# Optimization experiments

Hardware: AMD Instinct MI355X
Metric: run time of the kernel (lower is better)

Reference implementation:

```python
import jax, jax.numpy as jnp
import numpy as np
from jax import lax

B, T, D, U = 64, 2048, 512, 32


def setup_inputs() -> dict:
    key = jax.random.key(0)
    k1, k2, k3, k4 = jax.random.split(key, 4)
    x = jax.random.normal(k1, (B, T, D), dtype=jnp.float32)
    # sequence lengths in [1, T]
    nwords = jnp.maximum(jax.random.randint(k2, (B,), 0, T, dtype=jnp.int32), 1)
    kernel = jax.random.normal(k3, (D, U), dtype=jnp.float32) * 0.02
    chain_kernel = jax.random.normal(k4, (U, U), dtype=jnp.float32) * 0.02
    bias = jnp.zeros((U,), dtype=jnp.float32)
    return {"x": x, "nwords": nwords, "kernel": kernel,
            "chain_kernel": chain_kernel, "bias": bias}


def _crf_decode(logits, trans, lengths):
    """Viterbi decode. logits [B,T,U], trans [U,U], lengths [B] int.
    Returns (pred_ids [B,T] int32, best_score [B])."""
    Bb, Tt, Uu = logits.shape
    alpha0 = logits[:, 0]                       # [B,U]
    # valid[t-1, b] = (t < lengths[b]) for t = 1..T-1
    valid = (jnp.arange(1, Tt)[:, None] < lengths[None, :])  # [T-1, B]
    logits_rest = jnp.transpose(logits[:, 1:], (1, 0, 2))    # [T-1, B, U]
    tag_iota = jnp.arange(Uu, dtype=jnp.int32)

    def fwd_step(alpha, inp):
        logit_t, v = inp                        # [B,U], [B]
        scores = alpha[:, :, None] + trans[None, :, :]   # [B, U_prev, U_cur]
        bp = jnp.argmax(scores, axis=1).astype(jnp.int32)  # [B,U]
        new_alpha = jnp.max(scores, axis=1) + logit_t        # [B,U]
        new_alpha = jnp.where(v[:, None], new_alpha, alpha)
        bp = jnp.where(v[:, None], bp, tag_iota[None, :])    # identity at pads
        return new_alpha, bp

    final_alpha, bps = lax.scan(fwd_step, alpha0, (logits_rest, valid))
    # bps: [T-1, B, U]
    last_tag = jnp.argmax(final_alpha, axis=-1).astype(jnp.int32)  # [B]
    best_score = jnp.max(final_alpha, axis=-1)                     # [B]

    def back_step(tag, bp_t):
        prev_tag = jnp.take_along_axis(bp_t, tag[:, None], axis=1)[:, 0]
        return prev_tag, tag

    first_tag, tags_rest = lax.scan(back_step, last_tag, bps, reverse=True)
    # tags_rest[t-1] = tag at time t; first_tag = tag at time 0
    pred = jnp.concatenate([first_tag[None, :], tags_rest], axis=0)  # [T,B]
    return jnp.transpose(pred, (1, 0)), best_score


def reference(x, nwords, kernel, chain_kernel, bias):
    # dense projection (activation = linear, keras default)
    logits = jnp.einsum('btd,du->btu', x, kernel) + bias  # [B,T,U]
    pred_ids, best_score = _crf_decode(logits, chain_kernel, nwords)
    return pred_ids, best_score
```

## Files before the change

kernel.cpp:

```cpp
#include <hip/hip_runtime.h>

#define BB 64
#define TT 2048
#define DD 512
#define UU 32

#define NSEG 16
#define SEGLEN 128
#define SEGSH 7
#define NJ (NSEG - 1)

__device__ int g_ts[BB * NJ];
__device__ float g_c[BB * NJ];
__device__ float g_bound[BB * NSEG * 64];

__global__ __launch_bounds__(256) void k1_logits(const float* __restrict__ x,
                                                 const float* __restrict__ w,
                                                 const float* __restrict__ bias,
                                                 float* __restrict__ out) {
  __shared__ float xs[256 * 34];
  __shared__ float wsh[32 * 36];
  const int tid = threadIdx.x;
  const long row0 = (long)blockIdx.x * 256;
  const int tr = tid >> 2;
  const int tc = tid & 3;
  const int ubase = tc * 8;
  const int sr = tid >> 3;
  const int sc = (tid & 7) * 4;

  float acc[4][8];
#pragma unroll
  for (int i = 0; i < 4; ++i)
#pragma unroll
    for (int j = 0; j < 8; ++j) acc[i][j] = 0.0f;

  for (int kc = 0; kc < DD; kc += 32) {
#pragma unroll
    for (int p = 0; p < 8; ++p) {
      const int r = p * 32 + sr;
      const float4 v = *(const float4*)(x + (row0 + r) * DD + kc + sc);
      *(float2*)(&xs[r * 34 + sc]) = make_float2(v.x, v.y);
      *(float2*)(&xs[r * 34 + sc + 2]) = make_float2(v.z, v.w);
    }
    {
      const int k = tid >> 3;
      const int uu4 = (tid & 7) * 4;
      const float4 v = *(const float4*)(w + (size_t)(kc + k) * UU + uu4);
      *(float4*)(&wsh[k * 36 + uu4]) = v;
    }
    __syncthreads();
#pragma unroll
    for (int kp = 0; kp < 16; ++kp) {
      const int k = kp * 2;
      const float4 wa0 = *(const float4*)(&wsh[k * 36 + ubase]);
      const float4 wa1 = *(const float4*)(&wsh[k * 36 + ubase + 4]);
      const float4 wb0 = *(const float4*)(&wsh[(k + 1) * 36 + ubase]);
      const float4 wb1 = *(const float4*)(&wsh[(k + 1) * 36 + ubase + 4]);
      const float wva[8] = {wa0.x, wa0.y, wa0.z, wa0.w, wa1.x, wa1.y, wa1.z, wa1.w};
      const float wvb[8] = {wb0.x, wb0.y, wb0.z, wb0.w, wb1.x, wb1.y, wb1.z, wb1.w};
#pragma unroll
      for (int i = 0; i < 4; ++i) {
        const float2 xv2 = *(const float2*)(&xs[(tr + 64 * i) * 34 + k]);
#pragma unroll
        for (int j = 0; j < 8; ++j) acc[i][j] = fmaf(xv2.x, wva[j], acc[i][j]);
#pragma unroll
        for (int j = 0; j < 8; ++j) acc[i][j] = fmaf(xv2.y, wvb[j], acc[i][j]);
      }
    }
    __syncthreads();
  }
  float bv[8];
#pragma unroll
  for (int j = 0; j < 8; ++j) bv[j] = bias[ubase + j];
#pragma unroll
  for (int i = 0; i < 4; ++i) {
    const long row = row0 + tr + 64 * i;
    float4 o0, o1;
    o0.x = acc[i][0] + bv[0]; o0.y = acc[i][1] + bv[1];
    o0.z = acc[i][2] + bv[2]; o0.w = acc[i][3] + bv[3];
    o1.x = acc[i][4] + bv[4]; o1.y = acc[i][5] + bv[5];
    o1.z = acc[i][6] + bv[6]; o1.w = acc[i][7] + bv[7];
    *(float4*)(out + row * UU + ubase) = o0;
    *(float4*)(out + row * UU + ubase + 4) = o1;
  }
}


#define ROTF(S) \
  __int_as_float(__builtin_amdgcn_update_dpp(0, __float_as_int(P), 0x120 + (S), 0xF, 0xF, true))

#define K2_TREE                                                              \
    const float c0 = P + tvS[0];                                             \
    const float c1 = ROTF(1) + tvS[1];                                       \
    const float c2 = ROTF(2) + tvS[2];                                       \
    const float c3 = ROTF(3) + tvS[3];                                       \
    const float c4 = ROTF(4) + tvS[4];                                       \
    const float c5 = ROTF(5) + tvS[5];                                       \
    const float c6 = ROTF(6) + tvS[6];                                       \
    const float c7 = ROTF(7) + tvS[7];                                       \
    const float c8 = ROTF(8) + tvS[8];                                       \
    const float c9 = ROTF(9) + tvS[9];                                       \
    const float c10 = ROTF(10) + tvS[10];                                    \
    const float c11 = ROTF(11) + tvS[11];                                    \
    const float c12 = ROTF(12) + tvS[12];                                    \
    const float c13 = ROTF(13) + tvS[13];                                    \
    const float c14 = ROTF(14) + tvS[14];                                    \
    const float c15 = ROTF(15) + tvS[15];                                    \
    const float d0 = fmaxf(fmaxf(c0, c1), c2);                               \
    const float d1 = fmaxf(fmaxf(c3, c4), c5);                               \
    const float d2 = fmaxf(fmaxf(c6, c7), c8);                               \
    const float d3 = fmaxf(fmaxf(c9, c10), c11);                             \
    const float d4 = fmaxf(fmaxf(c12, c13), c14);                            \
    const float e0 = fmaxf(fmaxf(d0, d1), d2);                               \
    const float e1 = fmaxf(fmaxf(d3, d4), c15);                              \
    const float pm = fmaxf(e0, e1);

#if __has_builtin(__builtin_amdgcn_permlane32_swap) && __has_builtin(__builtin_amdgcn_permlane16_swap)
#define K2_HAVE_PERMLANE 1
typedef unsigned int v2u __attribute__((ext_vector_type(2)));

#define K2_FSTEP(tval, lg) do {                                              \
    K2_TREE                                                                  \
    v2u s32 = __builtin_amdgcn_permlane32_swap(__float_as_uint(pm),          \
                                               __float_as_uint(pm), false, false); \
    const float pd = fmaxf(__uint_as_float(s32.x), __uint_as_float(s32.y)) + (lg); \
    v2u s16 = __builtin_amdgcn_permlane16_swap(__float_as_uint(pd),          \
                                               __float_as_uint(pd), false, false); \
    const float cx = m16sel ? __uint_as_float(s16.x) : __uint_as_float(s16.y); \
    P = bit5v ? cx : pd;                                                     \
    base[(size_t)(tval) * UU + cstoS] = P;                                   \
  } while (0)

__device__ __forceinline__ float k2_mcomb(float P, const float* tvS) {
  K2_TREE
  v2u s32 = __builtin_amdgcn_permlane32_swap(__float_as_uint(pm),
                                             __float_as_uint(pm), false, false);
  return fmaxf(__uint_as_float(s32.x), __uint_as_float(s32.y));
}

#define K2_RUNSEG(A_, E_) do {                                               \
    int tcc = (A_);                                                          \
    _Pragma("unroll")                                                        \
    for (int i = 0; i < 16; ++i) {                                           \
      int r = (A_) + i; if (r > (E_)) r = (E_);                              \
      bufA[i] = base[(size_t)r * UU + tgtS];                                 \
    }                                                                        \
    _Pragma("unroll 1")                                                      \
    for (; tcc + 31 <= (E_); tcc += 32) {                                    \
      _Pragma("unroll")                                                      \
      for (int i = 0; i < 16; ++i) bufB[i] = base[(size_t)(tcc + 16 + i) * UU + tgtS]; \
      _Pragma("unroll")                                                      \
      for (int i = 0; i < 16; ++i) K2_FSTEP(tcc + i, bufA[i]);               \
      _Pragma("unroll")                                                      \
      for (int i = 0; i < 16; ++i) {                                         \
        int r = tcc + 32 + i; if (r > (E_)) r = (E_);                        \
        bufA[i] = base[(size_t)r * UU + tgtS];                               \
      }                                                                      \
      _Pragma("unroll")                                                      \
      for (int i = 0; i < 16; ++i) K2_FSTEP(tcc + 16 + i, bufB[i]);          \
    }                                                                        \
    const int rem = (E_) - tcc + 1;                                          \
    if (rem > 0) {                                                           \
      _Pragma("unroll")                                                      \
      for (int i = 0; i < 16; ++i) {                                         \
        int r = tcc + 16 + i; if (r > (E_)) r = (E_);                        \
        bufB[i] = base[(size_t)r * UU + tgtS];                               \
      }                                                                      \
      _Pragma("unroll")                                                      \
      for (int i = 0; i < 16; ++i) { if (i < rem) K2_FSTEP(tcc + i, bufA[i]); } \
      _Pragma("unroll")                                                      \
      for (int i = 0; i < 16; ++i) { if (16 + i < rem) K2_FSTEP(tcc + 16 + i, bufB[i]); } \
    }                                                                        \
  } while (0)
#endif

__global__ __launch_bounds__(64) void k2a_forward(float* __restrict__ lb,
                                                  const float* __restrict__ trans) {
  const int lane = threadIdx.x;
  const int q = lane & 15;
  const int bit4 = (lane >> 4) & 1;
  const int bit5v = (lane >> 5) & 1;
  const int hiS = bit4 ^ bit5v;
  const int tgtS = bit4 * 16 + q;
  const int cstoS = hiS * 16 + q;
  const int role = blockIdx.x >> 6;
  const int b = blockIdx.x & 63;

  const int probe = __builtin_amdgcn_update_dpp(0, q, 0x121, 0xF, 0xF, false);
  const bool dirp = (probe == ((q + 1) & 15));

  float tvS[16];
#pragma unroll
  for (int s = 0; s < 16; ++s) {
    const int rp = dirp ? ((q + s) & 15) : ((q - s) & 15);
    tvS[s] = trans[(hiS * 16 + rp) * UU + tgtS];
  }

  float* base = lb + (size_t)b * TT * UU;
  float bufA[16], bufB[16];

#ifdef K2_HAVE_PERMLANE
  v2u p32 = __builtin_amdgcn_permlane32_swap((unsigned)lane, (unsigned)lane, false, false);
  v2u p16 = __builtin_amdgcn_permlane16_swap((unsigned)lane, (unsigned)lane, false, false);
  const bool c32ok = ((int)p32.x == (lane ^ 32)) || ((int)p32.y == (lane ^ 32));
  const bool c16ok = ((int)p16.x == (lane ^ 16)) || ((int)p16.y == (lane ^ 16));
  const bool m16sel = ((int)p16.x == (lane ^ 16));
  const bool okSwap = (__ballot(c32ok) == ~0ull) && (__ballot(c16ok) == ~0ull);

  if (okSwap) {
    if (role == 0) {
      float P = base[cstoS];
      K2_RUNSEG(1, SEGLEN);
      g_bound[((b << 4) + 0) * 64 + lane] = P;
    } else {
      const int s0 = SEGLEN * role + 1;
      const int E = (role < NJ) ? (SEGLEN * (role + 1)) : (TT - 1);
      float P = base[(size_t)s0 * UU + cstoS];
      K2_RUNSEG(s0 + 1, E);
      g_bound[((b << 4) + role) * 64 + lane] = P;
    }
    return;
  }
#endif

  if (role != 0) return;
  {
    float tvD[16];
#pragma unroll
    for (int s = 0; s < 16; ++s) {
      const int rp = dirp ? ((q + s) & 15) : ((q - s) & 15);
      tvD[s] = trans[(bit4 * 16 + rp) * UU + cstoS];
    }
    const int idx32 = (lane ^ 32) << 2;
    const int idx48 = (lane ^ 48) << 2;
    float P = base[cstoS];

#define K2_BSTEP(tval, lg, TVHI, XIDX, SCOL) do {                            \
    const float g0 = P + (TVHI)[0];                                          \
    const float g1 = ROTF(1) + (TVHI)[1];                                    \
    const float g2 = ROTF(2) + (TVHI)[2];                                    \
    const float g3 = ROTF(3) + (TVHI)[3];                                    \
    const float g4 = ROTF(4) + (TVHI)[4];                                    \
    const float g5 = ROTF(5) + (TVHI)[5];                                    \
    const float g6 = ROTF(6) + (TVHI)[6];                                    \
    const float g7 = ROTF(7) + (TVHI)[7];                                    \
    const float g8 = ROTF(8) + (TVHI)[8];                                    \
    const float g9 = ROTF(9) + (TVHI)[9];                                    \
    const float g10 = ROTF(10) + (TVHI)[10];                                 \
    const float g11 = ROTF(11) + (TVHI)[11];                                 \
    const float g12 = ROTF(12) + (TVHI)[12];                                 \
    const float g13 = ROTF(13) + (TVHI)[13];                                 \
    const float g14 = ROTF(14) + (TVHI)[14];                                 \
    const float g15 = ROTF(15) + (TVHI)[15];                                 \
    const float h0 = fmaxf(fmaxf(g0, g1), g2);                               \
    const float h1 = fmaxf(fmaxf(g3, g4), g5);                               \
    const float h2 = fmaxf(fmaxf(g6, g7), g8);                               \
    const float h3 = fmaxf(fmaxf(g9, g10), g11);                             \
    const float h4 = fmaxf(fmaxf(g12, g13), g14);                            \
    const float k0 = fmaxf(fmaxf(h0, h1), h2);                               \
    const float k1 = fmaxf(fmaxf(h3, h4), g15);                              \
    const float pm2 = fmaxf(k0, k1);                                         \
    const int po = __builtin_amdgcn_ds_bpermute((XIDX), __float_as_int(pm2));\
    P = fmaxf(pm2, __int_as_float(po)) + (lg);                               \
    base[(size_t)(tval) * UU + (SCOL)] = P;                                  \
  } while (0)

#pragma unroll
    for (int i = 0; i < 16; ++i)
      bufA[i] = base[(size_t)(1 + i) * UU + ((i & 1) ? cstoS : tgtS)];
#pragma unroll 1
    for (int tc = 1; tc <= 1985; tc += 32) {
#pragma unroll
      for (int i = 0; i < 16; ++i)
        bufB[i] = base[(size_t)(tc + 16 + i) * UU + ((i & 1) ? cstoS : tgtS)];
#pragma unroll
      for (int i = 0; i < 16; ++i) {
        if ((i & 1) == 0) K2_BSTEP(tc + i, bufA[i], tvS, idx32, tgtS);
        else              K2_BSTEP(tc + i, bufA[i], tvD, idx48, cstoS);
      }
#pragma unroll
      for (int i = 0; i < 16; ++i)
        bufA[i] = base[(size_t)(tc + 32 + i) * UU + ((i & 1) ? cstoS : tgtS)];
#pragma unroll
      for (int i = 0; i < 16; ++i) {
        if ((i & 1) == 0) K2_BSTEP(tc + 16 + i, bufB[i], tvS, idx32, tgtS);
        else              K2_BSTEP(tc + 16 + i, bufB[i], tvD, idx48, cstoS);
      }
    }
#pragma unroll
    for (int i = 0; i < 16; ++i) {
      int r = 2033 + i; if (r > TT - 1) r = TT - 1;
      bufB[i] = base[(size_t)r * UU + ((i & 1) ? cstoS : tgtS)];
    }
#pragma unroll
    for (int i = 0; i < 16; ++i) {
      if ((i & 1) == 0) K2_BSTEP(2017 + i, bufA[i], tvS, idx32, tgtS);
      else              K2_BSTEP(2017 + i, bufA[i], tvD, idx48, cstoS);
    }
#pragma unroll
    for (int i = 0; i < 15; ++i) {
      if ((i & 1) == 0) K2_BSTEP(2033 + i, bufB[i], tvS, idx32, tgtS);
      else              K2_BSTEP(2033 + i, bufB[i], tvD, idx48, cstoS);
    }
  }
}

__global__ __launch_bounds__(64) void k2b_fixup(float* __restrict__ lb,
                                                const float* __restrict__ trans) {
  const int lane = threadIdx.x;
  const int b = blockIdx.x & 63;
  const int j = (blockIdx.x >> 6) + 1;
  const int q = lane & 15;
  const int bit4 = (lane >> 4) & 1;
  const int bit5v = (lane >> 5) & 1;
  const int hiS = bit4 ^ bit5v;
  const int tgtS = bit4 * 16 + q;
  const int cstoS = hiS * 16 + q;
  const int jr = SEGLEN * j + 1;
  const int segEnd = (j < NJ) ? (SEGLEN * (j + 1)) : (TT - 1);

  const int probe = __builtin_amdgcn_update_dpp(0, q, 0x121, 0xF, 0xF, false);
  const bool dirp = (probe == ((q + 1) & 15));

  float tvS[16];
#pragma unroll
  for (int s = 0; s < 16; ++s) {
    const int rp = dirp ? ((q + s) & 15) : ((q - s) & 15);
    tvS[s] = trans[(hiS * 16 + rp) * UU + tgtS];
  }

#ifdef K2_HAVE_PERMLANE
  v2u p32 = __builtin_amdgcn_permlane32_swap((unsigned)lane, (unsigned)lane, false, false);
  v2u p16 = __builtin_amdgcn_permlane16_swap((unsigned)lane, (unsigned)lane, false, false);
  const bool c32ok = ((int)p32.x == (lane ^ 32)) || ((int)p32.y == (lane ^ 32));
  const bool c16ok = ((int)p16.x == (lane ^ 16)) || ((int)p16.y == (lane ^ 16));
  const bool m16sel = ((int)p16.x == (lane ^ 16));
  const bool okSwap = (__ballot(c32ok) == ~0ull) && (__ballot(c16ok) == ~0ull);
  if (!okSwap) {
    if (lane == 0) { g_ts[b * NJ + j - 1] = segEnd; g_c[b * NJ + j - 1] = 0.0f; }
    return;
  }

  float* base = lb + (size_t)b * TT * UU;
  const float TAU = 0.05f;

  float trueP = g_bound[((b << 4) + (j - 1)) * 64 + lane];
  const float specInit = base[(size_t)jr * UU + cstoS];
  const float lgj = base[(size_t)jr * UU + tgtS];
  { float P = trueP; K2_FSTEP(jr, lgj); trueP = P; }
  float specP = specInit;

  float ring[4];
#pragma unroll
  for (int i = 0; i < 4; ++i) {
    int r = jr + 1 + i; if (r > segEnd) r = segEnd;
    ring[i] = base[(size_t)r * UU + cstoS];
  }
  int ts_rec = segEnd; float c_rec = 0.0f;
#pragma unroll 1
  for (int t = jr + 1; t <= segEnd; ++t) {
    const float specRow = ring[(t - (jr + 1)) & 3];
    const int pf = t + 4;
    if (pf <= segEnd) ring[(t - (jr + 1)) & 3] = base[(size_t)pf * UU + cstoS];
    const float Mt = k2_mcomb(trueP, tvS);
    const float Ms = k2_mcomb(specP, tvS);
    const float d = Mt - Ms;
    v2u s16d = __builtin_amdgcn_permlane16_swap(__float_as_uint(d),
                                                __float_as_uint(d), false, false);
    const float dx = m16sel ? __uint_as_float(s16d.x) : __uint_as_float(s16d.y);
    const float dsel = bit5v ? dx : d;
    const float nt = specRow + dsel;
    base[(size_t)t * UU + cstoS] = nt;
    const float dref = __uint_as_float(
        (unsigned)__builtin_amdgcn_readfirstlane(__float_as_int(d)));
    const bool uni = (__ballot(fabsf(d - dref) <= TAU) == ~0ull);
    trueP = nt;
    specP = specRow;
    if (uni) { ts_rec = t; c_rec = dref; break; }
  }
  if (lane == 0) { g_ts[b * NJ + j - 1] = ts_rec; g_c[b * NJ + j - 1] = c_rec; }
#else
  if (lane == 0) { g_ts[b * NJ + j - 1] = segEnd; g_c[b * NJ + j - 1] = 0.0f; }
#endif
}

__global__ __launch_bounds__(256) void k3_bp(const float* __restrict__ lb,
                                             const float* __restrict__ trans,
                                             const int* __restrict__ nwords,
                                             unsigned char* __restrict__ bp) {
  __shared__ float as[129 * 32];
  __shared__ float ts[32 * 32];
  const int b = blockIdx.x >> 4;
  const int c = blockIdx.x & 15;
  const int t0 = 128 * c;
  const int tid = threadIdx.x;
  const float* base = lb + (size_t)b * TT * UU;
  const int nw = nwords[b];

  float C[NSEG];
  int TS[NSEG];
  C[0] = 0.0f; TS[0] = 0;
#pragma unroll
  for (int j = 1; j <= NJ; ++j) {
    C[j] = C[j - 1] + g_c[b * NJ + j - 1];
    TS[j] = g_ts[b * NJ + j - 1];
  }

  for (int idx = tid; idx < 129 * 32; idx += 256) {
    const int gidx = (t0 - 1) * 32 + idx;
    float v = 0.0f;
    if (gidx >= 0 && gidx < TT * UU) {
      const int row = (t0 - 1) + (idx >> 5);
      const int jj = (row - 1) >> SEGSH;
      float off = 0.0f;
      if (jj >= 1) off = (row <= TS[jj]) ? C[jj - 1] : C[jj];
      v = base[gidx] + off;
    }
    as[idx] = v;
  }
  for (int idx = tid; idx < 1024; idx += 256) ts[idx] = trans[idx];
  __syncthreads();

  const int u = tid & 31;
  const int tg = tid >> 5;
  unsigned char* bpu = bp + ((size_t)b * 32 + u) * TT;

#pragma unroll 1
  for (int qq = 0; qq < 4; ++qq) {
    const int tl0 = tg * 16 + qq * 4;
    unsigned int pack = 0;
#pragma unroll
    for (int e = 0; e < 4; ++e) {
      const int tl = tl0 + e;
      const int t = t0 + tl;
      int idx;
      if (t >= 1 && t < nw) {
        float m = as[tl * 32 + 0] + ts[0 * 32 + u];
        idx = 0;
#pragma unroll
        for (int v = 1; v < 32; ++v) {
          const float cv = as[tl * 32 + v] + ts[v * 32 + u];
          if (cv > m) { m = cv; idx = v; }
        }
      } else {
        idx = u;
      }
      pack |= ((unsigned int)idx) << (8 * e);
    }
    *(unsigned int*)(bpu + t0 + tl0) = pack;
  }
}

__global__ __launch_bounds__(64) void k4_backtrace(const float* __restrict__ lb,
                                                   const unsigned char* __restrict__ bp,
                                                   const int* __restrict__ nwords,
                                                   int* __restrict__ pred,
                                                   float* __restrict__ score) {
  const int b = blockIdx.x;
  const int lane = threadIdx.x;
  const int u = lane & 31;
  const int h = lane >> 5;
  const int nw = nwords[b];

  float off = 0.0f;
  {
    const int row = nw - 1;
    const int jj = (row - 1) >> SEGSH;
    if (jj >= 1) {
      float Cacc = 0.0f;
      float Cprev = 0.0f;
#pragma unroll
      for (int j = 1; j <= NJ; ++j) {
        Cprev = Cacc;
        Cacc += g_c[b * NJ + j - 1];
        if (j == jj) off = (row <= g_ts[b * NJ + j - 1]) ? Cprev : Cacc;
      }
    }
  }

  const float a = lb[((size_t)b * TT + (nw - 1)) * UU + u] + off;
  float m = a;
#pragma unroll
  for (int s = 32; s; s >>= 1) m = fmaxf(m, __shfl_xor(m, s));
  if (lane == 0) score[b] = m;
  const unsigned long long mask = __ballot(lane < 32 && a == m);
  int tag = __ffsll((unsigned long long)mask) - 1;
  tag = __builtin_amdgcn_readfirstlane(tag);

  int* predb = pred + b * TT;
  for (int p = nw - 1 + lane; p < TT; p += 64) predb[p] = tag;
  if (nw < 2) return;

  const unsigned char* bpb = bp + (size_t)b * 32 * TT;
  const int pcmax = (nw - 2) >> 6;
  const int thi_top = nw - 1;

  int wprev0 = 0;
  {
    const int toff = (pcmax + 1) * 64;
    if (toff < TT) wprev0 = *(const int*)(bpb + (size_t)u * TT + toff);
  }

  for (int pc = pcmax; pc >= 0; --pc) {
    int wreg[8];
#pragma unroll
    for (int j = 0; j < 8; ++j)
      wreg[j] = *(const int*)(bpb + (size_t)u * TT + pc * 64 + 4 * (h * 8 + j));
    int predv = 0;

    if (pc == pcmax) {
      const int thi = thi_top;
      if (pc * 64 + 64 <= thi) {
        const int val = __builtin_amdgcn_readlane(wprev0, tag);
        tag = __builtin_amdgcn_readfirstlane(val & 0xFF);
        if (lane == 63) predv = tag;
      }
#pragma unroll
      for (int lt = 63; lt >= 1; --lt) {
        if (pc * 64 + lt <= thi) {
          const int d = lt >> 2, byte = lt & 3;
          const int hs = d >> 3, j = d & 7;
          const int val = __builtin_amdgcn_readlane(wreg[j], hs * 32 + tag);
          tag = __builtin_amdgcn_readfirstlane((val >> (8 * byte)) & 0xFF);
          if (lane == lt - 1) predv = tag;
        }
      }
      const int lim = thi - pc * 64;
      if (lane < lim) predb[pc * 64 + lane] = predv;
    } else {
      {
        const int val = __builtin_amdgcn_readlane(wprev0, tag);
        tag = __builtin_amdgcn_readfirstlane(val & 0xFF);
        if (lane == 63) predv = tag;
      }
#pragma unroll
      for (int lt = 63; lt >= 1; --lt) {
        const int d = lt >> 2, byte = lt & 3;
        const int hs = d >> 3, j = d & 7;
        const int val = __builtin_amdgcn_readlane(wreg[j], hs * 32 + tag);
        tag = __builtin_amdgcn_readfirstlane((val >> (8 * byte)) & 0xFF);
        if (lane == lt - 1) predv = tag;
      }
      predb[pc * 64 + lane] = predv;
    }
    wprev0 = wreg[0];
  }
}

extern "C" void kernel_launch(void* const* d_in, const int* in_sizes, int n_in,
                              void* d_out, int out_size, void* d_ws, size_t ws_size,
                              hipStream_t stream) {
  const float* x = (const float*)d_in[0];
  const int* nwords = (const int*)d_in[1];
  const float* kern = (const float*)d_in[2];
  const float* chain = (const float*)d_in[3];
  const float* bias = (const float*)d_in[4];

  float* logits = (float*)d_ws;
  unsigned char* bp = (unsigned char*)d_ws + (size_t)BB * TT * UU * 4;

  int* pred = (int*)d_out;
  float* score = (float*)d_out + (size_t)BB * TT;

  k1_logits<<<dim3(512), dim3(256), 0, stream>>>(x, kern, bias, logits);
  k2a_forward<<<dim3(NSEG * 64), dim3(64), 0, stream>>>(logits, chain);
  k2b_fixup<<<dim3(NJ * 64), dim3(64), 0, stream>>>(logits, chain);
  k3_bp<<<dim3(BB * 16), dim3(256), 0, stream>>>(logits, chain, nwords, bp);
  k4_backtrace<<<dim3(BB), dim3(64), 0, stream>>>(logits, bp, nwords, pred, score);
}
```

Measured before the change: 172.6 us.

## Save raw segment logits so fixup recomputes the forward recursion without dual max-combines

```diff
diff --git a/kernel.cpp b/kernel.cpp
--- a/kernel.cpp
+++ b/kernel.cpp
@@ -9,10 +9,12 @@
 #define SEGLEN 128
 #define SEGSH 7
 #define NJ (NSEG - 1)
+#define WSAVE 96
 
 __device__ int g_ts[BB * NJ];
 __device__ float g_c[BB * NJ];
 __device__ float g_bound[BB * NSEG * 64];
+__device__ float g_slog[(size_t)BB * NJ * WSAVE * 64];
 
 __global__ __launch_bounds__(256) void k1_logits(const float* __restrict__ x,
                                                  const float* __restrict__ w,
@@ -216,7 +218,25 @@
       const int s0 = SEGLEN * role + 1;
       const int E = (role < NJ) ? (SEGLEN * (role + 1)) : (TT - 1);
       float P = base[(size_t)s0 * UU + cstoS];
-      K2_RUNSEG(s0 + 1, E);
+      {
+        float* sp = &g_slog[(((size_t)b * NJ + (role - 1)) * WSAVE) * 64 + lane];
+        const int A = s0 + 1;
+#pragma unroll
+        for (int i = 0; i < 16; ++i) bufA[i] = base[(size_t)(A + i) * UU + tgtS];
+#pragma unroll 1
+        for (int ch = 0; ch < 3; ++ch) {
+          const int t0c = A + ch * 32;
+#pragma unroll
+          for (int i = 0; i < 16; ++i) bufB[i] = base[(size_t)(t0c + 16 + i) * UU + tgtS];
+#pragma unroll
+          for (int i = 0; i < 16; ++i) { sp[(size_t)(ch * 32 + i) * 64] = bufA[i]; K2_FSTEP(t0c + i, bufA[i]); }
+#pragma unroll
+          for (int i = 0; i < 16; ++i) bufA[i] = base[(size_t)(t0c + 32 + i) * UU + tgtS];
+#pragma unroll
+          for (int i = 0; i < 16; ++i) { sp[(size_t)(ch * 32 + 16 + i) * 64] = bufB[i]; K2_FSTEP(t0c + 16 + i, bufB[i]); }
+        }
+      }
+      K2_RUNSEG(s0 + 1 + WSAVE, E);
       g_bound[((b << 4) + role) * 64 + lane] = P;
     }
     return;
@@ -344,39 +364,64 @@
   float* base = lb + (size_t)b * TT * UU;
   const float TAU = 0.05f;
 
-  float trueP = g_bound[((b << 4) + (j - 1)) * 64 + lane];
-  const float specInit = base[(size_t)jr * UU + cstoS];
+  float P = g_bound[((b << 4) + (j - 1)) * 64 + lane];
   const float lgj = base[(size_t)jr * UU + tgtS];
-  { float P = trueP; K2_FSTEP(jr, lgj); trueP = P; }
-  float specP = specInit;
+  K2_FSTEP(jr, lgj);
+
+  const float* sp = &g_slog[(((size_t)b * NJ + (j - 1)) * WSAVE) * 64 + lane];
 
   float ring[4];
 #pragma unroll
-  for (int i = 0; i < 4; ++i) {
-    int r = jr + 1 + i; if (r > segEnd) r = segEnd;
-    ring[i] = base[(size_t)r * UU + cstoS];
-  }
-  int ts_rec = segEnd; float c_rec = 0.0f;
+  for (int i = 0; i < 4; ++i) ring[i] = base[(size_t)(jr + 1 + i) * UU + cstoS];
+
+  int ts_rec = segEnd; float c_rec = 0.0f; bool done = false;
+  float lastSpec = 0.0f;
+
 #pragma unroll 1
-  for (int t = jr + 1; t <= segEnd; ++t) {
-    const float specRow = ring[(t - (jr + 1)) & 3];
+  for (int w = 0; w < WSAVE; ++w) {
+    const int t = jr + 1 + w;
+    const float specRow = ring[w & 3];
     const int pf = t + 4;
-    if (pf <= segEnd) ring[(t - (jr + 1)) & 3] = base[(size_t)pf * UU + cstoS];
-    const float Mt = k2_mcomb(trueP, tvS);
-    const float Ms = k2_mcomb(specP, tvS);
-    const float d = Mt - Ms;
-    v2u s16d = __builtin_amdgcn_permlane16_swap(__float_as_uint(d),
-                                                __float_as_uint(d), false, false);
-    const float dx = m16sel ? __uint_as_float(s16d.x) : __uint_as_float(s16d.y);
-    const float dsel = bit5v ? dx : d;
-    const float nt = specRow + dsel;
-    base[(size_t)t * UU + cstoS] = nt;
+    if (pf <= segEnd) ring[w & 3] = base[(size_t)pf * UU + cstoS];
+    const float lg = sp[(size_t)w * 64];
+    K2_FSTEP(t, lg);
+    const float d = P - specRow;
     const float dref = __uint_as_float(
         (unsigned)__builtin_amdgcn_readfirstlane(__float_as_int(d)));
     const bool uni = (__ballot(fabsf(d - dref) <= TAU) == ~0ull);
-    trueP = nt;
-    specP = specRow;
-    if (uni) { ts_rec = t; c_rec = dref; break; }
+    lastSpec = specRow;
+    if (uni) { ts_rec = t; c_rec = dref; done = true; break; }
+  }
+
+  if (!done) {
+    float trueP = P;
+    float specP = lastSpec;
+#pragma unroll
+    for (int i = 0; i < 4; ++i) {
+      int r = jr + WSAVE + 1 + i; if (r > segEnd) r = segEnd;
+      ring[i] = base[(size_t)r * UU + cstoS];
+    }
+#pragma unroll 1
+    for (int t = jr + WSAVE + 1; t <= segEnd; ++t) {
+      const float specRow = ring[(t - (jr + WSAVE + 1)) & 3];
+      const int pf = t + 4;
+      if (pf <= segEnd) ring[(t - (jr + WSAVE + 1)) & 3] = base[(size_t)pf * UU + cstoS];
+      const float Mt = k2_mcomb(trueP, tvS);
+      const float Ms = k2_mcomb(specP, tvS);
+      const float d = Mt - Ms;
+      v2u s16d = __builtin_amdgcn_permlane16_swap(__float_as_uint(d),
+                                                  __float_as_uint(d), false, false);
+      const float dx = m16sel ? __uint_as_float(s16d.x) : __uint_as_float(s16d.y);
+      const float dsel = bit5v ? dx : d;
+      const float nt = specRow + dsel;
+      base[(size_t)t * UU + cstoS] = nt;
+      const float dref = __uint_as_float(
+          (unsigned)__builtin_amdgcn_readfirstlane(__float_as_int(d)));
+      const bool uni = (__ballot(fabsf(d - dref) <= TAU) == ~0ull);
+      trueP = nt;
+      specP = specRow;
+      if (uni) { ts_rec = t; c_rec = dref; break; }
+    }
   }
   if (lane == 0) { g_ts[b * NJ + j - 1] = ts_rec; g_c[b * NJ + j - 1] = c_rec; }
 #else
```

Result: slower. 178.1 us (+3.1%).
